# Optimization experiments

Measured on AMD Instinct MI355X. Metric: run time of the kernel, lower is better.

Reference implementation:

```python
import jax, jax.numpy as jnp
import numpy as np

B, L, DM = 4, 2048, 1024
DI, DS, DR, K = 2 * DM, 16, 64, 4  # d_inner, d_state, dt_rank, d_conv


def setup_inputs() -> dict:
    key = jax.random.key(0)
    ks = jax.random.split(key, 10)
    # dt bias init as in Mamba: inv-softplus of dt ~ LogUniform(1e-3, 0.1)
    dt = jnp.exp(jax.random.uniform(ks[7], (DI,)) * (np.log(0.1) - np.log(1e-3)) + np.log(1e-3))
    dt = jnp.clip(dt, 1e-4, None)
    dt_proj_b = dt + jnp.log(-jnp.expm1(-dt))
    # A_log init: log(1..d_state) broadcast over d_inner
    A_log = jnp.log(jnp.broadcast_to(jnp.arange(1, DS + 1, dtype=jnp.float32), (DI, DS)))
    return {
        "hidden": jax.random.normal(ks[0], (B, L, DM), jnp.float32),
        "in_proj_w": jax.random.normal(ks[1], (2 * DI, DM), jnp.float32) * 0.02,
        "conv_w": jax.random.normal(ks[2], (DI, 1, K), jnp.float32) * 0.2,
        "conv_b": jax.random.normal(ks[3], (DI,), jnp.float32) * 0.02,
        "x_proj_w": jax.random.normal(ks[4], (DR + 2 * DS, DI), jnp.float32) * 0.02,
        "dt_proj_w": jax.random.normal(ks[5], (DI, DR), jnp.float32) * (DR ** -0.5),
        "dt_proj_b": dt_proj_b,
        "A_log": A_log,
        "D_param": jnp.ones((DI,), jnp.float32),
        "out_proj_w": jax.random.normal(ks[6], (DM, DI), jnp.float32) * 0.02,
    }


def reference(hidden, in_proj_w, conv_w, conv_b, x_proj_w, dt_proj_w, dt_proj_b, A_log, D_param, out_proj_w):
    b, l, dm = hidden.shape
    di = in_proj_w.shape[0] // 2
    ds = A_log.shape[1]
    dr = dt_proj_w.shape[1]
    k = conv_w.shape[-1]

    # in_proj (no bias): (b,l,2*di)
    xz = jnp.einsum('bld,ed->ble', hidden, in_proj_w)
    x, z = jnp.split(xz, 2, axis=-1)

    # causal depthwise conv1d over time + SiLU
    xt = x.transpose(0, 2, 1)  # (b, di, l)
    xc = jax.lax.conv_general_dilated(
        xt, conv_w, window_strides=(1,), padding=[(k - 1, 0)],
        feature_group_count=di, dimension_numbers=('NCH', 'OIH', 'NCH'))
    xc = jax.nn.silu(xc + conv_b[None, :, None])
    u = xc.transpose(0, 2, 1)  # (b, l, di)

    # input-dependent dt, B, C
    x_dbl = jnp.einsum('bld,ed->ble', u, x_proj_w)  # (b,l,dr+2*ds)
    dt, Bm, Cm = jnp.split(x_dbl, [dr, dr + ds], axis=-1)
    delta = jax.nn.softplus(jnp.einsum('blr,dr->bld', dt, dt_proj_w) + dt_proj_b)  # (b,l,di)

    A = -jnp.exp(A_log)  # (di, ds)

    def step(h, inp):
        dlt, Bt, Ct, ut = inp  # (b,di), (b,ds), (b,ds), (b,di)
        dA = jnp.exp(dlt[..., None] * A)               # (b,di,ds)
        h = dA * h + (dlt * ut)[..., None] * Bt[:, None, :]
        y = jnp.einsum('bdn,bn->bd', h, Ct)
        return h, y

    h0 = jnp.zeros((b, di, ds), hidden.dtype)
    xs = (delta.transpose(1, 0, 2), Bm.transpose(1, 0, 2),
          Cm.transpose(1, 0, 2), u.transpose(1, 0, 2))
    _, ys = jax.lax.scan(step, h0, xs)  # ys: (l,b,di)

    y = ys.transpose(1, 0, 2) + u * D_param  # skip connection
    y = y * jax.nn.silu(z)                   # gate
    return jnp.einsum('bld,od->blo', y, out_proj_w)
```

## Files before the change

### kernel.cpp

```cpp
#include <hip/hip_runtime.h>
#include <hip/hip_bf16.h>
#include <math.h>

#define BB 4
#define LL 2048
#define DM 1024
#define DI 2048
#define DS 16
#define DR 64
#define KC 4
#define TT (BB * LL)
#define NC 32
#define CL (LL / NC)
#define SK 8

typedef __hip_bfloat16 bf16;
typedef short bf16x8 __attribute__((ext_vector_type(8)));
typedef short short8 __attribute__((ext_vector_type(8)));
typedef float f32x4 __attribute__((ext_vector_type(4)));
typedef float float4v __attribute__((ext_vector_type(4)));

__device__ __forceinline__ float cvt(float v) { return v; }
__device__ __forceinline__ float cvt(bf16 v) { return __bfloat162float(v); }
__device__ __forceinline__ float bf2f(short s) {
  union { short s; bf16 h; } c; c.s = s; return __bfloat162float(c.h);
}
__device__ __forceinline__ void stv(float* p, float v) { *p = v; }
__device__ __forceinline__ void stv(bf16* p, float v) { *p = __float2bfloat16(v); }
__device__ __forceinline__ short f2bf(float f) {
  union { bf16 h; short s; } u_; u_.h = __float2bfloat16(f); return u_.s;
}

__device__ __forceinline__ void loadcvt16(const float* p, short* d) {
#pragma unroll
  for (int i = 0; i < 4; ++i) {
    float4v v = ((const float4v*)p)[i];
#pragma unroll
    for (int j = 0; j < 4; ++j) d[i * 4 + j] = f2bf(v[j]);
  }
}
__device__ __forceinline__ void loadcvt16(const bf16* p, short* d) {
  ((short8*)d)[0] = ((const short8*)p)[0];
  ((short8*)d)[1] = ((const short8*)p)[1];
}

template <typename TA, typename TC, int EPI>
__global__ __launch_bounds__(256) void gemm_mfma(
    const TA* __restrict__ A, int lda,
    const float* __restrict__ W, int ldw,
    const float* __restrict__ bias,
    TC* __restrict__ C, int ldc, int Kd) {
  __shared__ short As[128 * 40];
  __shared__ short Bs[128 * 40];
  int tid = threadIdx.x;
  int bm = blockIdx.y * 128, bn = blockIdx.x * 128;

  int r = tid >> 1, hh = (tid & 1) * 16;
  const TA* ga = A + (size_t)(bm + r) * lda + hh;
  const float* gw = W + (size_t)(bn + r) * ldw + hh;

  int wave = tid >> 6, lane = tid & 63;
  int wm = (wave >> 1) * 64, wn = (wave & 1) * 64;
  int lr = lane & 15, kg = lane >> 4;

  f32x4 acc[4][4] = {};

  for (int k0 = 0; k0 < Kd; k0 += 32) {
    short abuf[16], wbuf[16];
    loadcvt16(ga + k0, abuf);
    loadcvt16(gw + k0, wbuf);
    __syncthreads();
    ((short8*)&As[r * 40 + hh])[0] = ((short8*)abuf)[0];
    ((short8*)&As[r * 40 + hh])[1] = ((short8*)abuf)[1];
    ((short8*)&Bs[r * 40 + hh])[0] = ((short8*)wbuf)[0];
    ((short8*)&Bs[r * 40 + hh])[1] = ((short8*)wbuf)[1];
    __syncthreads();

    bf16x8 af[4], bfr[4];
#pragma unroll
    for (int i = 0; i < 4; ++i)
      af[i] = *(const bf16x8*)&As[(wm + i * 16 + lr) * 40 + kg * 8];
#pragma unroll
    for (int j = 0; j < 4; ++j)
      bfr[j] = *(const bf16x8*)&Bs[(wn + j * 16 + lr) * 40 + kg * 8];
#pragma unroll
    for (int i = 0; i < 4; ++i)
#pragma unroll
      for (int j = 0; j < 4; ++j)
        acc[i][j] = __builtin_amdgcn_mfma_f32_16x16x32_bf16(af[i], bfr[j], acc[i][j], 0, 0, 0);
  }

#pragma unroll
  for (int i = 0; i < 4; ++i) {
    int row0 = bm + wm + i * 16 + kg * 4;
#pragma unroll
    for (int j = 0; j < 4; ++j) {
      int col = bn + wn + j * 16 + lr;
#pragma unroll
      for (int rr = 0; rr < 4; ++rr) {
        float v = acc[i][j][rr];
        if (EPI == 1) {
          v += bias[col];
          v = (v > 20.f) ? v : log1pf(expf(v));
        }
        stv(&C[(size_t)(row0 + rr) * ldc + col], v);
      }
    }
  }
}

__device__ __forceinline__ float* stslot(bf16* xz, int idx) {
  int t = idx >> 10, j = idx & 1023;
  return (float*)((char*)xz + (size_t)t * 8192) + j;
}
#define SUMD_BASE (8192 * NC * DS)

__global__ __launch_bounds__(256) void xproj_splitk(
    const bf16* __restrict__ u, const float* __restrict__ W,
    bf16* __restrict__ xz) {
  __shared__ short As[128 * 40];
  __shared__ short Bs[96 * 40];
  int tid = threadIdx.x;
  int bm = blockIdx.x * 128;
  int sk = blockIdx.y;
  int kb = sk * (DI / SK);

  int r = tid >> 1, hh = (tid & 1) * 16;
  const bf16* ga = u + (size_t)(bm + r) * DI + kb + hh;
  const float* gw = W + (size_t)r * DI + kb + hh;

  int wave = tid >> 6, lane = tid & 63;
  int wm = wave * 32;
  int lr = lane & 15, kg = lane >> 4;

  f32x4 acc[2][6] = {};

  for (int k0 = 0; k0 < DI / SK; k0 += 32) {
    short abuf[16], wbuf[16];
    loadcvt16(ga + k0, abuf);
    if (r < 96) loadcvt16(gw + k0, wbuf);
    __syncthreads();
    ((short8*)&As[r * 40 + hh])[0] = ((short8*)abuf)[0];
    ((short8*)&As[r * 40 + hh])[1] = ((short8*)abuf)[1];
    if (r < 96) {
      ((short8*)&Bs[r * 40 + hh])[0] = ((short8*)wbuf)[0];
      ((short8*)&Bs[r * 40 + hh])[1] = ((short8*)wbuf)[1];
    }
    __syncthreads();

    bf16x8 af[2], bfr[6];
#pragma unroll
    for (int i = 0; i < 2; ++i)
      af[i] = *(const bf16x8*)&As[(wm + i * 16 + lr) * 40 + kg * 8];
#pragma unroll
    for (int j = 0; j < 6; ++j)
      bfr[j] = *(const bf16x8*)&Bs[(j * 16 + lr) * 40 + kg * 8];
#pragma unroll
    for (int i = 0; i < 2; ++i)
#pragma unroll
      for (int j = 0; j < 6; ++j)
        acc[i][j] = __builtin_amdgcn_mfma_f32_16x16x32_bf16(af[i], bfr[j], acc[i][j], 0, 0, 0);
  }

#pragma unroll
  for (int i = 0; i < 2; ++i) {
#pragma unroll
    for (int j = 0; j < 6; ++j) {
      int col = j * 16 + lr;
#pragma unroll
      for (int rr = 0; rr < 4; ++rr) {
        int row = bm + wm + i * 16 + kg * 4 + rr;
        *stslot(xz, (sk * 8192 + row) * 96 + col) = acc[i][j][rr];
      }
    }
  }
}

__global__ __launch_bounds__(256) void xproj_reduce(
    bf16* __restrict__ xz, float* __restrict__ xdbl) {
  int gid = blockIdx.x * 256 + threadIdx.x;
  float s = 0.f;
#pragma unroll
  for (int sk = 0; sk < SK; ++sk)
    s += *stslot(xz, sk * (8192 * 96) + gid);
  xdbl[gid] = s;
}

__global__ __launch_bounds__(256) void conv_silu(
    const bf16* __restrict__ xz, const float* __restrict__ cw,
    const float* __restrict__ cb, bf16* __restrict__ u) {
  int t = blockIdx.x;
  int d0 = threadIdx.x * 8;
  int l = t & (LL - 1);

  float acc[8];
  float4v c0 = *(const float4v*)&cb[d0];
  float4v c1 = *(const float4v*)&cb[d0 + 4];
#pragma unroll
  for (int j = 0; j < 4; ++j) { acc[j] = c0[j]; acc[4 + j] = c1[j]; }

  float wv[32];
  const float4v* wp = (const float4v*)&cw[d0 * 4];
#pragma unroll
  for (int q = 0; q < 8; ++q) {
    float4v v = wp[q];
#pragma unroll
    for (int j = 0; j < 4; ++j) wv[q * 4 + j] = v[j];
  }

#pragma unroll
  for (int k = 0; k < KC; ++k) {
    int lt = l - (KC - 1) + k;
    if (lt >= 0) {
      short8 xv = *(const short8*)&xz[(size_t)(t - (KC - 1) + k) * (2 * DI) + d0];
#pragma unroll
      for (int q = 0; q < 8; ++q)
        acc[q] = fmaf(bf2f(xv[q]), wv[q * 4 + k], acc[q]);
    }
  }

  short8 ov;
#pragma unroll
  for (int q = 0; q < 8; ++q) {
    float s = acc[q] / (1.f + __expf(-acc[q]));
    ov[q] = f2bf(s);
  }
  *(short8*)&u[(size_t)t * DI + d0] = ov;
}

__global__ __launch_bounds__(256) void scan_local(
    const bf16* __restrict__ delta, const bf16* __restrict__ u,
    const float* __restrict__ xdbl, bf16* __restrict__ xz,
    const float* __restrict__ A_log) {
  int g = blockIdx.x * 256 + threadIdx.x;
  int d = g & (DI - 1);
  int b = (g >> 11) & (BB - 1);
  int c = g >> 13;
  int chain = (b << 11) | d;

  float Aj[DS];
  const float4v* Ap = (const float4v*)&A_log[d * DS];
#pragma unroll
  for (int i = 0; i < 4; ++i) {
    float4v v = Ap[i];
#pragma unroll
    for (int j = 0; j < 4; ++j) Aj[i * 4 + j] = -__expf(v[j]);
  }

  float h[DS];
#pragma unroll
  for (int s = 0; s < DS; ++s) h[s] = 0.f;
  float sd = 0.f;
  int t0 = b * LL + c * CL;

  for (int i = 0; i < CL; ++i) {
    int t = t0 + i;
    float dlt = cvt(delta[(size_t)t * DI + d]);
    float ut = cvt(u[(size_t)t * DI + d]);
    const float4v* Bp = (const float4v*)&xdbl[(size_t)t * (DR + 2 * DS) + DR];
    float Bv[DS];
#pragma unroll
    for (int q = 0; q < 4; ++q) {
      float4v v = Bp[q];
#pragma unroll
      for (int j = 0; j < 4; ++j) Bv[q * 4 + j] = v[j];
    }
    float du = dlt * ut;
    sd += dlt;
#pragma unroll
    for (int s = 0; s < DS; ++s)
      h[s] = fmaf(__expf(dlt * Aj[s]), h[s], du * Bv[s]);
  }

  float4v* hv = (float4v*)stslot(xz, (chain * NC + c) * DS);
#pragma unroll
  for (int q = 0; q < 4; ++q) {
    float4v v;
#pragma unroll
    for (int j = 0; j < 4; ++j) v[j] = h[q * 4 + j];
    hv[q] = v;
  }
  *stslot(xz, SUMD_BASE + chain * NC + c) = sd;
}

__global__ __launch_bounds__(256) void scan_fix(
    bf16* __restrict__ xz, const float* __restrict__ A_log) {
  int lane = threadIdx.x & 15;
  int chain = blockIdx.x * 16 + (threadIdx.x >> 4);
  int d = chain & (DI - 1);
  float Aj = -__expf(A_log[d * DS + lane]);
  float carry = 0.f;
  for (int c = 0; c < NC; ++c) {
    float* hp = stslot(xz, (chain * NC + c) * DS + lane);
    float sd = *stslot(xz, SUMD_BASE + chain * NC + c);
    float he = *hp;
    *hp = carry;
    carry = fmaf(__expf(Aj * sd), carry, he);
  }
}

__global__ __launch_bounds__(256) void scan_final(
    const bf16* __restrict__ delta, bf16* __restrict__ u,
    const float* __restrict__ xdbl, bf16* __restrict__ xz,
    const float* __restrict__ A_log, const float* __restrict__ Dp) {
  int g = blockIdx.x * 256 + threadIdx.x;
  int d = g & (DI - 1);
  int b = (g >> 11) & (BB - 1);
  int c = g >> 13;
  int chain = (b << 11) | d;

  float Aj[DS];
  const float4v* Ap = (const float4v*)&A_log[d * DS];
#pragma unroll
  for (int i = 0; i < 4; ++i) {
    float4v v = Ap[i];
#pragma unroll
    for (int j = 0; j < 4; ++j) Aj[i * 4 + j] = -__expf(v[j]);
  }
  float Dd = Dp[d];

  float h[DS];
  const float4v* hv = (const float4v*)stslot(xz, (chain * NC + c) * DS);
#pragma unroll
  for (int q = 0; q < 4; ++q) {
    float4v v = hv[q];
#pragma unroll
    for (int j = 0; j < 4; ++j) h[q * 4 + j] = v[j];
  }

  int t0 = b * LL + c * CL;
  for (int i = 0; i < CL; ++i) {
    int t = t0 + i;
    float dlt = cvt(delta[(size_t)t * DI + d]);
    float ut = cvt(u[(size_t)t * DI + d]);
    const float4v* Bp = (const float4v*)&xdbl[(size_t)t * (DR + 2 * DS) + DR];
    float BC[2 * DS];
#pragma unroll
    for (int q = 0; q < 8; ++q) {
      float4v v = Bp[q];
#pragma unroll
      for (int j = 0; j < 4; ++j) BC[q * 4 + j] = v[j];
    }
    float du = dlt * ut;
    float yp = 0.f;
#pragma unroll
    for (int s = 0; s < DS; ++s) {
      h[s] = fmaf(__expf(dlt * Aj[s]), h[s], du * BC[s]);
      yp = fmaf(h[s], BC[DS + s], yp);
    }
    float zt = cvt(xz[(size_t)t * (2 * DI) + DI + d]);
    float gte = zt / (1.f + __expf(-zt));
    stv(&u[(size_t)t * DI + d], (yp + ut * Dd) * gte);
  }
}

extern "C" void kernel_launch(void* const* d_in, const int* in_sizes, int n_in,
                              void* d_out, int out_size, void* d_ws, size_t ws_size,
                              hipStream_t stream) {
  const float* hidden    = (const float*)d_in[0];
  const float* in_proj_w = (const float*)d_in[1];
  const float* conv_w    = (const float*)d_in[2];
  const float* conv_b    = (const float*)d_in[3];
  const float* x_proj_w  = (const float*)d_in[4];
  const float* dt_proj_w = (const float*)d_in[5];
  const float* dt_proj_b = (const float*)d_in[6];
  const float* A_log     = (const float*)d_in[7];
  const float* D_param   = (const float*)d_in[8];
  const float* out_proj_w= (const float*)d_in[9];
  float* out = (float*)d_out;

  size_t need = (size_t)TT * 4096 * sizeof(bf16) + (size_t)TT * DI * sizeof(bf16)
              + (size_t)TT * (DR + 2 * DS) * sizeof(float) + (size_t)TT * DI * sizeof(bf16);
  if (ws_size < need) return;

  bf16* xz     = (bf16*)d_ws;
  bf16* u      = xz + (size_t)TT * 2 * DI;
  float* xdbl  = (float*)(u + (size_t)TT * DI);
  bf16* delta  = (bf16*)(xdbl + (size_t)TT * (DR + 2 * DS));

  dim3 blk(256);

  gemm_mfma<float, bf16, 0><<<dim3(4096 / 128, TT / 128), blk, 0, stream>>>(
      hidden, DM, in_proj_w, DM, nullptr, xz, 2 * DI, DM);

  conv_silu<<<dim3(TT), blk, 0, stream>>>(xz, conv_w, conv_b, u);

  xproj_splitk<<<dim3(TT / 128, SK), blk, 0, stream>>>(u, x_proj_w, xz);
  xproj_reduce<<<dim3(TT * 96 / 256), blk, 0, stream>>>(xz, xdbl);

  gemm_mfma<float, bf16, 1><<<dim3(DI / 128, TT / 128), blk, 0, stream>>>(
      xdbl, DR + 2 * DS, dt_proj_w, DR, dt_proj_b, delta, DI, DR);

  scan_local<<<dim3(8192 * NC / 256), blk, 0, stream>>>(delta, u, xdbl, xz, A_log);
  scan_fix<<<dim3(8192 / 16), blk, 0, stream>>>(xz, A_log);
  scan_final<<<dim3(8192 * NC / 256), blk, 0, stream>>>(delta, u, xdbl, xz, A_log, D_param);

  gemm_mfma<bf16, float, 0><<<dim3(DM / 128, TT / 128), blk, 0, stream>>>(
      u, DI, out_proj_w, DI, nullptr, out, DM, DI);
}
```

Before: 609.1 us.

## Pre-convert GEMM operands to bf16 and load tiles via direct global-to-LDS

Adds a bf16 conversion kernel for hidden, in_proj and out_proj weights, and a new MFMA GEMM that fetches tiles with global_load_lds straight into shared memory. in_proj and out_proj now use this GEMM instead of converting fp32 on the fly in the register load path. Converted buffers reuse workspace regions (u, delta) that are dead at those points. The cost is extra conversion passes and a single-buffered loop with two barriers per k-step.

Measured after the change: 535.2 us. 12.1% less time.

```diff
diff --git a/kernel.cpp b/kernel.cpp
--- a/kernel.cpp
+++ b/kernel.cpp
@@ -29,6 +29,85 @@
 __device__ __forceinline__ void stv(bf16* p, float v) { *p = __float2bfloat16(v); }
 __device__ __forceinline__ short f2bf(float f) {
   union { bf16 h; short s; } u_; u_.h = __float2bfloat16(f); return u_.s;
+}
+
+__device__ __forceinline__ void gld16(const bf16* g, bf16* l) {
+  __builtin_amdgcn_global_load_lds(
+      (const __attribute__((address_space(1))) void*)g,
+      (__attribute__((address_space(3))) void*)l, 16, 0, 0);
+}
+
+__global__ __launch_bounds__(256) void cvt_bf16(
+    const float* __restrict__ src, bf16* __restrict__ dst, int n8) {
+  int i = blockIdx.x * 256 + threadIdx.x;
+  if (i >= n8) return;
+  const float4v* s = (const float4v*)(src + (size_t)i * 8);
+  float4v v0 = s[0], v1 = s[1];
+  short8 o;
+#pragma unroll
+  for (int j = 0; j < 4; ++j) { o[j] = f2bf(v0[j]); o[4 + j] = f2bf(v1[j]); }
+  *(short8*)(dst + (size_t)i * 8) = o;
+}
+
+template <typename TC>
+__global__ __launch_bounds__(256) void gemm_bf16(
+    const bf16* __restrict__ A, int lda,
+    const bf16* __restrict__ W, int ldw,
+    TC* __restrict__ C, int ldc, int Kd) {
+  __shared__ bf16 As[128 * 32];
+  __shared__ bf16 Bs[128 * 32];
+  int tid = threadIdx.x;
+  int bm = blockIdx.y * 128, bn = blockIdx.x * 128;
+  int wave = tid >> 6, lane = tid & 63;
+  int wm = (wave >> 1) * 64, wn = (wave & 1) * 64;
+  int lr = lane & 15, kg = lane >> 4;
+
+  int srow = wave * 16 + (lane >> 2);
+  int kc = (lane & 3) * 8;
+  const bf16* gA0 = A + (size_t)(bm + srow) * lda + kc;
+  const bf16* gA1 = gA0 + (size_t)64 * lda;
+  const bf16* gW0 = W + (size_t)(bn + srow) * ldw + kc;
+  const bf16* gW1 = gW0 + (size_t)64 * ldw;
+  bf16* lA0 = &As[wave * 512];
+  bf16* lA1 = &As[2048 + wave * 512];
+  bf16* lB0 = &Bs[wave * 512];
+  bf16* lB1 = &Bs[2048 + wave * 512];
+
+  f32x4 acc[4][4] = {};
+
+  for (int k0 = 0; k0 < Kd; k0 += 32) {
+    __syncthreads();
+    gld16(gA0 + k0, lA0);
+    gld16(gA1 + k0, lA1);
+    gld16(gW0 + k0, lB0);
+    gld16(gW1 + k0, lB1);
+    __syncthreads();
+
+    bf16x8 af[4], bfr[4];
+#pragma unroll
+    for (int i = 0; i < 4; ++i)
+      af[i] = *(const bf16x8*)&As[(wm + i * 16 + lr) * 32 + kg * 8];
+#pragma unroll
+    for (int j = 0; j < 4; ++j)
+      bfr[j] = *(const bf16x8*)&Bs[(wn + j * 16 + lr) * 32 + kg * 8];
+#pragma unroll
+    for (int i = 0; i < 4; ++i)
+#pragma unroll
+      for (int j = 0; j < 4; ++j)
+        acc[i][j] = __builtin_amdgcn_mfma_f32_16x16x32_bf16(af[i], bfr[j], acc[i][j], 0, 0, 0);
+  }
+
+#pragma unroll
+  for (int i = 0; i < 4; ++i) {
+    int row0 = bm + wm + i * 16 + kg * 4;
+#pragma unroll
+    for (int j = 0; j < 4; ++j) {
+      int col = bn + wn + j * 16 + lr;
+#pragma unroll
+      for (int rr = 0; rr < 4; ++rr)
+        stv(&C[(size_t)(row0 + rr) * ldc + col], acc[i][j][rr]);
+    }
+  }
 }
 
 __device__ __forceinline__ void loadcvt16(const float* p, short* d) {
@@ -378,10 +457,17 @@
   float* xdbl  = (float*)(u + (size_t)TT * DI);
   bf16* delta  = (bf16*)(xdbl + (size_t)TT * (DR + 2 * DS));
 
+  bf16* hbf  = u;
+  bf16* wbf  = u + (size_t)TT * DM;
+  bf16* opbf = delta;
+
   dim3 blk(256);
 
-  gemm_mfma<float, bf16, 0><<<dim3(4096 / 128, TT / 128), blk, 0, stream>>>(
-      hidden, DM, in_proj_w, DM, nullptr, xz, 2 * DI, DM);
+  cvt_bf16<<<dim3(TT * DM / 8 / 256), blk, 0, stream>>>(hidden, hbf, TT * DM / 8);
+  cvt_bf16<<<dim3(2 * DI * DM / 8 / 256), blk, 0, stream>>>(in_proj_w, wbf, 2 * DI * DM / 8);
+
+  gemm_bf16<bf16><<<dim3(4096 / 128, TT / 128), blk, 0, stream>>>(
+      hbf, DM, wbf, DM, xz, 2 * DI, DM);
 
   conv_silu<<<dim3(TT), blk, 0, stream>>>(xz, conv_w, conv_b, u);
 
@@ -395,6 +481,8 @@
   scan_fix<<<dim3(8192 / 16), blk, 0, stream>>>(xz, A_log);
   scan_final<<<dim3(8192 * NC / 256), blk, 0, stream>>>(delta, u, xdbl, xz, A_log, D_param);
 
-  gemm_mfma<bf16, float, 0><<<dim3(DM / 128, TT / 128), blk, 0, stream>>>(
-      u, DI, out_proj_w, DI, nullptr, out, DM, DI);
-}
+  cvt_bf16<<<dim3(DM * DI / 8 / 256), blk, 0, stream>>>(out_proj_w, opbf, DM * DI / 8);
+
+  gemm_bf16<float><<<dim3(DM / 128, TT / 128), blk, 0, stream>>>(
+      u, DI, opbf, DI, out, DM, DI);
+}
```
